# Kernel optimization log

Measured on AMD Instinct MI355X. Metric: run time of the kernel, lower is better.

Reference implementation:

```python
import jax, jax.numpy as jnp
import numpy as np

N_NODES = 1_000_000
N_EDGES = 32_000_000
N_GRAPHS = 1024
N_LAYERS = 8


def setup_inputs() -> dict:
    key = jax.random.key(0)
    k1, k2, k3, k4, k5, k6, k7 = jax.random.split(key, 7)
    x = jnp.ones((N_NODES, 1), dtype=jnp.float32)
    src = jax.random.randint(k1, (N_EDGES,), 0, N_NODES, dtype=jnp.int32)
    dst = jax.random.randint(k2, (N_EDGES,), 0, N_NODES, dtype=jnp.int32)
    edge_weight = jax.random.uniform(k3, (N_EDGES,), dtype=jnp.float32)
    graph_ids = jnp.sort(jax.random.randint(k4, (N_NODES,), 0, N_GRAPHS, dtype=jnp.int32))
    W_neigh = jax.random.normal(k5, (N_LAYERS, 1, 1), dtype=jnp.float32)
    b_neigh = jax.random.normal(k6, (N_LAYERS, 1), dtype=jnp.float32)
    W_self = jax.random.normal(k7, (N_LAYERS, 1, 1), dtype=jnp.float32)
    return {"x": x, "src": src, "dst": dst, "edge_weight": edge_weight,
            "graph_ids": graph_ids, "W_neigh": W_neigh, "b_neigh": b_neigh,
            "W_self": W_self}


def reference(x, src, dst, edge_weight, graph_ids, W_neigh, b_neigh, W_self):
    # FixedNet forward with conv_type='GraphConvWL', concat_features=True.
    h = x
    xs = [h]
    for l in range(N_LAYERS):
        # GraphConv(norm='none'): sum over in-edges of src features * edge_weight,
        # then linear weight + bias.
        msg = h[src] * edge_weight[:, None]            # [E, 1]
        agg = jax.ops.segment_sum(msg, dst, num_segments=N_NODES)  # [N, 1]
        neigh = agg @ W_neigh[l] + b_neigh[l]          # conv_from_neigh
        self_f = h @ W_self[l]                          # conv_from_self (no bias)
        h = jax.nn.relu(neigh + self_f)
        xs.append(h)
    hcat = jnp.concatenate(xs, axis=1)                  # [N, N_LAYERS+1]
    # dgl.sum_nodes: per-graph sum over batched graphs
    hg = jax.ops.segment_sum(hcat, graph_ids, num_segments=N_GRAPHS)  # [G, 9]
    return hg
```

## Files before the change

kernel.cpp:

```cpp
#include <hip/hip_runtime.h>

#define N_NODES  1000000
#define N_EDGES  32000000
#define N_GRAPHS 1024
#define N_LAYERS 8
#define OUT_COLS (N_LAYERS + 1)

#define BKT_SHIFT 11
#define BKT_NODES 2048
#define NBKT      489
#define NBKT_PAD  512
#define SCAT_BLOCKS 256
#define SCAT_THREADS 1024
#define SCAT_CHUNK  (N_EDGES / SCAT_BLOCKS)

__device__ inline void seg_accum(int gid, float val, float* __restrict__ out, int col) {
    int g0 = __shfl(gid, 0);
    if (__all(gid == g0)) {
        #pragma unroll
        for (int off = 32; off > 0; off >>= 1)
            val += __shfl_down(val, off);
        if ((threadIdx.x & 63) == 0)
            atomicAdd(&out[g0 * OUT_COLS + col], val);
    } else {
        atomicAdd(&out[gid * OUT_COLS + col], val);
    }
}


__global__ void count_kernel(const int4* __restrict__ dst4, unsigned* __restrict__ g_count) {
    __shared__ unsigned hist[NBKT_PAD];
    for (int j = threadIdx.x; j < NBKT_PAD; j += blockDim.x) hist[j] = 0u;
    __syncthreads();
    int stride = gridDim.x * blockDim.x;
    for (int t = blockIdx.x * blockDim.x + threadIdx.x; t < N_EDGES / 4; t += stride) {
        int4 d = dst4[t];
        atomicAdd(&hist[((unsigned)d.x) >> BKT_SHIFT], 1u);
        atomicAdd(&hist[((unsigned)d.y) >> BKT_SHIFT], 1u);
        atomicAdd(&hist[((unsigned)d.z) >> BKT_SHIFT], 1u);
        atomicAdd(&hist[((unsigned)d.w) >> BKT_SHIFT], 1u);
    }
    __syncthreads();
    for (int j = threadIdx.x; j < NBKT_PAD; j += blockDim.x)
        if (hist[j]) atomicAdd(&g_count[j], hist[j]);
}

__global__ void scan_kernel(const unsigned* __restrict__ g_count,
                            unsigned* __restrict__ g_base,
                            unsigned* __restrict__ g_cursor) {
    __shared__ unsigned s[NBKT_PAD];
    int t = threadIdx.x;
    unsigned c = g_count[t];
    s[t] = c;
    __syncthreads();
    for (int off = 1; off < NBKT_PAD; off <<= 1) {
        unsigned v = (t >= off) ? s[t - off] : 0u;
        __syncthreads();
        s[t] += v;
        __syncthreads();
    }
    unsigned incl = s[t];
    g_base[t]   = incl - c;
    g_cursor[t] = incl - c;
    if (t == NBKT_PAD - 1) g_base[NBKT_PAD] = incl;
}

__global__ void scatter_kernel(const int* __restrict__ src,
                               const int* __restrict__ dst,
                               const float* __restrict__ ew,
                               unsigned* __restrict__ g_cursor,
                               unsigned long long* __restrict__ recs) {
    __shared__ unsigned lhist[NBKT_PAD];
    __shared__ unsigned lbase[NBKT_PAD];
    int e0 = blockIdx.x * SCAT_CHUNK;
    int e1 = e0 + SCAT_CHUNK;
    for (int j = threadIdx.x; j < NBKT_PAD; j += blockDim.x) lhist[j] = 0u;
    __syncthreads();
    for (int e = e0 + threadIdx.x; e < e1; e += blockDim.x)
        atomicAdd(&lhist[((unsigned)dst[e]) >> BKT_SHIFT], 1u);
    __syncthreads();
    for (int j = threadIdx.x; j < NBKT_PAD; j += blockDim.x) {
        unsigned c = lhist[j];
        lbase[j] = c ? atomicAdd(&g_cursor[j], c) : 0u;
    }
    __syncthreads();
    for (int j = threadIdx.x; j < NBKT_PAD; j += blockDim.x) lhist[j] = 0u;
    __syncthreads();
    for (int e = e0 + threadIdx.x; e < e1; e += blockDim.x) {
        unsigned d = (unsigned)dst[e];
        unsigned b = d >> BKT_SHIFT;
        unsigned loc = atomicAdd(&lhist[b], 1u);
        unsigned pos = lbase[b] + loc;
        unsigned hi  = ((unsigned)src[e]) | ((d & (BKT_NODES - 1u)) << 20);
        recs[pos] = ((unsigned long long)hi << 32) | (unsigned)__float_as_uint(ew[e]);
    }
}

__global__ __launch_bounds__(1024) void sort_kernel(
        const unsigned long long* __restrict__ recs_in,
        const unsigned* __restrict__ g_base,
        unsigned long long* __restrict__ recs_out,
        unsigned* __restrict__ row_ptr) {
    __shared__ unsigned cnt[BKT_NODES];
    __shared__ unsigned ps[1024];
    int b = blockIdx.x;
    int t = threadIdx.x;
    int e0 = (int)g_base[b];
    int e1 = (int)g_base[b + 1];
    cnt[t] = 0u; cnt[t + 1024] = 0u;
    __syncthreads();
    for (int e = e0 + t; e < e1; e += 1024)
        atomicAdd(&cnt[(unsigned)(recs_in[e] >> 52)], 1u);
    __syncthreads();
    unsigned c0 = cnt[2 * t], c1 = cnt[2 * t + 1];
    ps[t] = c0 + c1;
    __syncthreads();
    for (int off = 1; off < 1024; off <<= 1) {
        unsigned u = (t >= off) ? ps[t - off] : 0u;
        __syncthreads();
        ps[t] += u;
        __syncthreads();
    }
    unsigned exPair = ps[t] - (c0 + c1);
    unsigned ex0 = exPair, ex1 = exPair + c0;
    int nbase = b << BKT_SHIFT;
    int n0 = nbase + 2 * t, n1 = n0 + 1;
    if (n0 <= N_NODES) row_ptr[n0] = (unsigned)e0 + ex0;
    if (n1 <= N_NODES) row_ptr[n1] = (unsigned)e0 + ex1;
    __syncthreads();
    cnt[2 * t] = ex0; cnt[2 * t + 1] = ex1;
    __syncthreads();
    for (int e = e0 + t; e < e1; e += 1024) {
        unsigned long long r = recs_in[e];
        unsigned j = (unsigned)(r >> 52);
        unsigned pos = (unsigned)e0 + atomicAdd(&cnt[j], 1u);
        recs_out[pos] = r;
    }
}


__global__ void init_kernel(const float* __restrict__ x,
                            const int* __restrict__ gids,
                            float* __restrict__ h0,
                            float* __restrict__ out) {
    int i = blockIdx.x * blockDim.x + threadIdx.x;
    if (i >= N_NODES) return;
    float v = x[i];
    h0[i] = v;
    seg_accum(gids[i], v, out, 0);
}

__global__ __launch_bounds__(256) void layer_kernel(
        const unsigned long long* __restrict__ recs,
        const unsigned* __restrict__ row_ptr,
        const float* __restrict__ h_old,
        float* __restrict__ h_new,
        const int* __restrict__ gids,
        const float* __restrict__ Wn,
        const float* __restrict__ bn,
        const float* __restrict__ Ws,
        float* __restrict__ out,
        int l) {
    int n = blockIdx.x * 256 + threadIdx.x;
    if (n >= N_NODES) return;
    int s = (int)row_ptr[n];
    int e = (int)row_ptr[n + 1];
    float a0 = 0.0f, a1 = 0.0f;
    int i = s;
    for (; i + 2 <= e; i += 2) {
        unsigned long long r0 = recs[i];
        unsigned long long r1 = recs[i + 1];
        a0 = fmaf(h_old[(unsigned)(r0 >> 32) & 0xFFFFFu], __uint_as_float((unsigned)r0), a0);
        a1 = fmaf(h_old[(unsigned)(r1 >> 32) & 0xFFFFFu], __uint_as_float((unsigned)r1), a1);
    }
    if (i < e) {
        unsigned long long r0 = recs[i];
        a0 = fmaf(h_old[(unsigned)(r0 >> 32) & 0xFFFFFu], __uint_as_float((unsigned)r0), a0);
    }
    float a = a0 + a1;
    float hn = fmaxf(fmaf(a, Wn[l], fmaf(h_old[n], Ws[l], bn[l])), 0.0f);
    h_new[n] = hn;
    seg_accum(gids[n], hn, out, l + 1);
}


__global__ void bkt_layer_kernel(const unsigned long long* __restrict__ recs,
                                 const unsigned* __restrict__ g_base,
                                 const float* __restrict__ h_old,
                                 float* __restrict__ h_new,
                                 const int* __restrict__ gids,
                                 const float* __restrict__ Wn,
                                 const float* __restrict__ bn,
                                 const float* __restrict__ Ws,
                                 float* __restrict__ out,
                                 int l) {
    __shared__ float agg[BKT_NODES];
    int b = blockIdx.x;
    for (int j = threadIdx.x; j < BKT_NODES; j += blockDim.x) agg[j] = 0.0f;
    __syncthreads();
    int e0 = (int)g_base[b];
    int e1 = (int)g_base[b + 1];
    for (int e = e0 + threadIdx.x; e < e1; e += blockDim.x) {
        unsigned long long rec = __builtin_nontemporal_load(&recs[e]);
        unsigned hi = (unsigned)(rec >> 32);
        float w  = __uint_as_float((unsigned)rec);
        float hv = h_old[hi & 0xFFFFFu];
        atomicAdd(&agg[hi >> 20], hv * w);
    }
    __syncthreads();
    float wn = Wn[l], bb = bn[l], ws = Ws[l];
    int nbase = b << BKT_SHIFT;
    for (int j = threadIdx.x; j < BKT_NODES; j += blockDim.x) {
        int n = nbase + j;
        if (n < N_NODES) {
            float hn = fmaxf(fmaf(agg[j], wn, fmaf(h_old[n], ws, bb)), 0.0f);
            h_new[n] = hn;
            seg_accum(gids[n], hn, out, l + 1);
        }
    }
}


__global__ void fb_init_kernel(const float* __restrict__ x, const int* __restrict__ gids,
                               float* __restrict__ h, float* __restrict__ agg,
                               float* __restrict__ out) {
    int i = blockIdx.x * blockDim.x + threadIdx.x;
    if (i >= N_NODES) return;
    float v = x[i];
    h[i] = v; agg[i] = 0.0f;
    seg_accum(gids[i], v, out, 0);
}
__global__ void fb_edge_kernel(const int4* __restrict__ src4, const int4* __restrict__ dst4,
                               const float4* __restrict__ ew4, const float* __restrict__ h,
                               float* __restrict__ agg) {
    int t = blockIdx.x * blockDim.x + threadIdx.x;
    if (t >= N_EDGES / 4) return;
    int4 s = src4[t]; int4 d = dst4[t]; float4 w = ew4[t];
    atomicAdd(&agg[d.x], h[s.x] * w.x);
    atomicAdd(&agg[d.y], h[s.y] * w.y);
    atomicAdd(&agg[d.z], h[s.z] * w.z);
    atomicAdd(&agg[d.w], h[s.w] * w.w);
}
__global__ void fb_node_kernel(float* __restrict__ h, float* __restrict__ agg,
                               const int* __restrict__ gids, const float* __restrict__ Wn,
                               const float* __restrict__ bn, const float* __restrict__ Ws,
                               float* __restrict__ out, int l) {
    int i = blockIdx.x * blockDim.x + threadIdx.x;
    if (i >= N_NODES) return;
    float a = agg[i]; agg[i] = 0.0f;
    float hv = h[i];
    float hn = fmaxf(fmaf(a, Wn[l], fmaf(hv, Ws[l], bn[l])), 0.0f);
    h[i] = hn;
    seg_accum(gids[i], hn, out, l + 1);
}


extern "C" void kernel_launch(void* const* d_in, const int* in_sizes, int n_in,
                              void* d_out, int out_size, void* d_ws, size_t ws_size,
                              hipStream_t stream) {
    const float* x   = (const float*)d_in[0];
    const int*   src = (const int*)  d_in[1];
    const int*   dst = (const int*)  d_in[2];
    const float* ew  = (const float*)d_in[3];
    const int*   gid = (const int*)  d_in[4];
    const float* Wn  = (const float*)d_in[5];
    const float* bn  = (const float*)d_in[6];
    const float* Ws  = (const float*)d_in[7];
    float* out = (float*)d_out;

    hipMemsetAsync(d_out, 0, (size_t)out_size * sizeof(float), stream);

    const int BT = 256;
    const int nb = (N_NODES + BT - 1) / BT;

    size_t need1 = (size_t)N_EDGES * 8 * 2
                 + (size_t)(N_NODES + 2) * 4
                 + (size_t)N_NODES * 4 * 2
                 + (size_t)(NBKT_PAD * 3 + 16) * 4;
    size_t need2 = (size_t)N_EDGES * 8
                 + (size_t)N_NODES * 4 * 2
                 + (size_t)(NBKT_PAD * 3 + 16) * 4;

    if (ws_size >= need1) {
        char* p = (char*)d_ws;
        unsigned long long* recs_tmp = (unsigned long long*)p;  p += (size_t)N_EDGES * 8;
        unsigned long long* recs     = (unsigned long long*)p;  p += (size_t)N_EDGES * 8;
        unsigned* row_ptr  = (unsigned*)p;                      p += (size_t)(N_NODES + 2) * 4;
        float*    h0       = (float*)p;                         p += (size_t)N_NODES * 4;
        float*    h1       = (float*)p;                         p += (size_t)N_NODES * 4;
        unsigned* g_count  = (unsigned*)p;                      p += NBKT_PAD * 4;
        unsigned* g_cursor = (unsigned*)p;                      p += NBKT_PAD * 4;
        unsigned* g_base   = (unsigned*)p;                      p += (NBKT_PAD + 1) * 4;

        hipMemsetAsync(g_count, 0, NBKT_PAD * 2 * sizeof(unsigned), stream);

        count_kernel  <<<2048, 256, 0, stream>>>((const int4*)dst, g_count);
        scan_kernel   <<<1, NBKT_PAD, 0, stream>>>(g_count, g_base, g_cursor);
        scatter_kernel<<<SCAT_BLOCKS, SCAT_THREADS, 0, stream>>>(src, dst, ew, g_cursor, recs_tmp);
        sort_kernel   <<<NBKT, 1024, 0, stream>>>(recs_tmp, g_base, recs, row_ptr);

        init_kernel<<<nb, BT, 0, stream>>>(x, gid, h0, out);

        float* ha = h0;
        float* hb = h1;
        for (int l = 0; l < N_LAYERS; ++l) {
            layer_kernel<<<nb, BT, 0, stream>>>(recs, row_ptr, ha, hb,
                                                gid, Wn, bn, Ws, out, l);
            float* t = ha; ha = hb; hb = t;
        }
        return;
    }

    if (ws_size >= need2) {
        char* p = (char*)d_ws;
        unsigned long long* recs = (unsigned long long*)p;  p += (size_t)N_EDGES * 8;
        float*    h0       = (float*)p;                     p += (size_t)N_NODES * 4;
        float*    h1       = (float*)p;                     p += (size_t)N_NODES * 4;
        unsigned* g_count  = (unsigned*)p;                  p += NBKT_PAD * 4;
        unsigned* g_cursor = (unsigned*)p;                  p += NBKT_PAD * 4;
        unsigned* g_base   = (unsigned*)p;                  p += (NBKT_PAD + 1) * 4;

        hipMemsetAsync(g_count, 0, NBKT_PAD * 2 * sizeof(unsigned), stream);

        count_kernel  <<<2048, 256, 0, stream>>>((const int4*)dst, g_count);
        scan_kernel   <<<1, NBKT_PAD, 0, stream>>>(g_count, g_base, g_cursor);
        scatter_kernel<<<SCAT_BLOCKS, SCAT_THREADS, 0, stream>>>(src, dst, ew, g_cursor, recs);

        init_kernel<<<nb, BT, 0, stream>>>(x, gid, h0, out);

        float* ha = h0;
        float* hb = h1;
        for (int l = 0; l < N_LAYERS; ++l) {
            bkt_layer_kernel<<<NBKT, 512, 0, stream>>>(recs, g_base, ha, hb,
                                                       gid, Wn, bn, Ws, out, l);
            float* t = ha; ha = hb; hb = t;
        }
        return;
    }

    float* h   = (float*)d_ws;
    float* agg = (float*)d_ws + N_NODES;
    const int eb = (N_EDGES / 4 + BT - 1) / BT;
    fb_init_kernel<<<nb, BT, 0, stream>>>(x, gid, h, agg, out);
    for (int l = 0; l < N_LAYERS; ++l) {
        fb_edge_kernel<<<eb, BT, 0, stream>>>(
            (const int4*)src, (const int4*)dst, (const float4*)ew, h, agg);
        fb_node_kernel<<<nb, BT, 0, stream>>>(h, agg, gid, Wn, bn, Ws, out, l);
    }
}
```

Measured before the change: 2.268 ms.

## Stage CSR edge records through LDS with coalesced block loads in layer kernel

The per-node CSR layer kernel now loads each block's contiguous edge-record range cooperatively into shared memory in coalesced chunks, then each thread walks its own row from LDS. This replaces strided per-thread global reads of the records. Global loads and stores are marked nontemporal, and the block size drops to 128. The count kernel also spreads its shared histogram across 4 replicas to reduce atomic contention. The cost is extra syncthreads and a 36KB LDS footprint that may limit occupancy.

```diff
diff --git a/kernel.cpp b/kernel.cpp
--- a/kernel.cpp
+++ b/kernel.cpp
@@ -13,6 +13,9 @@
 #define SCAT_BLOCKS 256
 #define SCAT_THREADS 1024
 #define SCAT_CHUNK  (N_EDGES / SCAT_BLOCKS)
+
+#define NPB  128
+#define CAP  4608
 
 __device__ inline void seg_accum(int gid, float val, float* __restrict__ out, int col) {
     int g0 = __shfl(gid, 0);
@@ -29,20 +32,23 @@
 
 
 __global__ void count_kernel(const int4* __restrict__ dst4, unsigned* __restrict__ g_count) {
-    __shared__ unsigned hist[NBKT_PAD];
-    for (int j = threadIdx.x; j < NBKT_PAD; j += blockDim.x) hist[j] = 0u;
-    __syncthreads();
+    __shared__ unsigned hist[NBKT_PAD * 4];
+    for (int j = threadIdx.x; j < NBKT_PAD * 4; j += blockDim.x) hist[j] = 0u;
+    __syncthreads();
+    int rep = threadIdx.x & 3;
     int stride = gridDim.x * blockDim.x;
     for (int t = blockIdx.x * blockDim.x + threadIdx.x; t < N_EDGES / 4; t += stride) {
         int4 d = dst4[t];
-        atomicAdd(&hist[((unsigned)d.x) >> BKT_SHIFT], 1u);
-        atomicAdd(&hist[((unsigned)d.y) >> BKT_SHIFT], 1u);
-        atomicAdd(&hist[((unsigned)d.z) >> BKT_SHIFT], 1u);
-        atomicAdd(&hist[((unsigned)d.w) >> BKT_SHIFT], 1u);
-    }
-    __syncthreads();
-    for (int j = threadIdx.x; j < NBKT_PAD; j += blockDim.x)
-        if (hist[j]) atomicAdd(&g_count[j], hist[j]);
+        atomicAdd(&hist[((((unsigned)d.x) >> BKT_SHIFT) << 2) + rep], 1u);
+        atomicAdd(&hist[((((unsigned)d.y) >> BKT_SHIFT) << 2) + rep], 1u);
+        atomicAdd(&hist[((((unsigned)d.z) >> BKT_SHIFT) << 2) + rep], 1u);
+        atomicAdd(&hist[((((unsigned)d.w) >> BKT_SHIFT) << 2) + rep], 1u);
+    }
+    __syncthreads();
+    for (int j = threadIdx.x; j < NBKT_PAD; j += blockDim.x) {
+        unsigned s = hist[4*j] + hist[4*j+1] + hist[4*j+2] + hist[4*j+3];
+        if (s) atomicAdd(&g_count[j], s);
+    }
 }
 
 __global__ void scan_kernel(const unsigned* __restrict__ g_count,
@@ -150,7 +156,7 @@
     seg_accum(gids[i], v, out, 0);
 }
 
-__global__ __launch_bounds__(256) void layer_kernel(
+__global__ __launch_bounds__(NPB) void layer_kernel(
         const unsigned long long* __restrict__ recs,
         const unsigned* __restrict__ row_ptr,
         const float* __restrict__ h_old,
@@ -161,26 +167,45 @@
         const float* __restrict__ Ws,
         float* __restrict__ out,
         int l) {
-    int n = blockIdx.x * 256 + threadIdx.x;
-    if (n >= N_NODES) return;
-    int s = (int)row_ptr[n];
-    int e = (int)row_ptr[n + 1];
+    __shared__ unsigned long long lds[CAP];
+    int t = threadIdx.x;
+    int nb0 = blockIdx.x * NPB;
+    int nend = nb0 + NPB; if (nend > N_NODES) nend = N_NODES;
+    int blk_e0 = (int)__builtin_nontemporal_load(&row_ptr[nb0]);
+    int blk_e1 = (int)__builtin_nontemporal_load(&row_ptr[nend]);
+    int n = nb0 + t;
+    int s = blk_e1, e = blk_e1;
+    if (n < N_NODES) {
+        s = (int)__builtin_nontemporal_load(&row_ptr[n]);
+        e = (int)__builtin_nontemporal_load(&row_ptr[n + 1]);
+    }
     float a0 = 0.0f, a1 = 0.0f;
-    int i = s;
-    for (; i + 2 <= e; i += 2) {
-        unsigned long long r0 = recs[i];
-        unsigned long long r1 = recs[i + 1];
-        a0 = fmaf(h_old[(unsigned)(r0 >> 32) & 0xFFFFFu], __uint_as_float((unsigned)r0), a0);
-        a1 = fmaf(h_old[(unsigned)(r1 >> 32) & 0xFFFFFu], __uint_as_float((unsigned)r1), a1);
-    }
-    if (i < e) {
-        unsigned long long r0 = recs[i];
-        a0 = fmaf(h_old[(unsigned)(r0 >> 32) & 0xFFFFFu], __uint_as_float((unsigned)r0), a0);
-    }
-    float a = a0 + a1;
-    float hn = fmaxf(fmaf(a, Wn[l], fmaf(h_old[n], Ws[l], bn[l])), 0.0f);
-    h_new[n] = hn;
-    seg_accum(gids[n], hn, out, l + 1);
+    for (int c0 = blk_e0; c0 < blk_e1; c0 += CAP) {
+        int c1 = c0 + CAP; if (c1 > blk_e1) c1 = blk_e1;
+        __syncthreads();
+        for (int i = c0 + t; i < c1; i += NPB)
+            lds[i - c0] = __builtin_nontemporal_load(&recs[i]);
+        __syncthreads();
+        int ls = s > c0 ? s : c0;
+        int le = e < c1 ? e : c1;
+        int i = ls;
+        for (; i + 2 <= le; i += 2) {
+            unsigned long long r0 = lds[i - c0];
+            unsigned long long r1 = lds[i + 1 - c0];
+            a0 = fmaf(h_old[(unsigned)(r0 >> 32) & 0xFFFFFu], __uint_as_float((unsigned)r0), a0);
+            a1 = fmaf(h_old[(unsigned)(r1 >> 32) & 0xFFFFFu], __uint_as_float((unsigned)r1), a1);
+        }
+        if (i < le) {
+            unsigned long long r0 = lds[i - c0];
+            a0 = fmaf(h_old[(unsigned)(r0 >> 32) & 0xFFFFFu], __uint_as_float((unsigned)r0), a0);
+        }
+    }
+    if (n < N_NODES) {
+        float hn = fmaxf(fmaf(a0 + a1, Wn[l], fmaf(h_old[n], Ws[l], bn[l])), 0.0f);
+        __builtin_nontemporal_store(hn, &h_new[n]);
+        int g = __builtin_nontemporal_load(&gids[n]);
+        seg_accum(g, hn, out, l + 1);
+    }
 }
 
 
@@ -303,9 +328,10 @@
 
         float* ha = h0;
         float* hb = h1;
+        const int lb = (N_NODES + NPB - 1) / NPB;
         for (int l = 0; l < N_LAYERS; ++l) {
-            layer_kernel<<<nb, BT, 0, stream>>>(recs, row_ptr, ha, hb,
-                                                gid, Wn, bn, Ws, out, l);
+            layer_kernel<<<lb, NPB, 0, stream>>>(recs, row_ptr, ha, hb,
+                                                 gid, Wn, bn, Ws, out, l);
             float* t = ha; ha = hb; hb = t;
         }
         return;
```

Measured after the change: 2.266 ms. About the same (-0.1%).
